# Kernel optimization log

Measured on AMD Instinct MI355X. Metric: run time of the kernel, lower is better.

Reference implementation:

```python
import jax, jax.numpy as jnp
import numpy as np

B, N, C, H, D = 1, 4096, 256, 8, 64  # batch, seq, channels, heads, head_dim


def setup_inputs() -> dict:
    key = jax.random.key(0)
    ks = jax.random.split(key, 11)
    s = 0.02
    return {
        "q_x": jax.random.normal(ks[0], (B, N, C), jnp.float32),
        "k_x": jax.random.normal(ks[1], (B, N, C), jnp.float32),
        "v_x": jax.random.normal(ks[2], (B, N, C), jnp.float32),
        "bias": jax.random.normal(ks[3], (B, 1, N, N), jnp.float32),
        "wq": jax.random.normal(ks[4], (H * D, C), jnp.float32) * s,
        "wk": jax.random.normal(ks[5], (H * D, C), jnp.float32) * s,
        "wv": jax.random.normal(ks[6], (H * D, C), jnp.float32) * s,
        "wg": jax.random.normal(ks[7], (H * D, C), jnp.float32) * s,
        "bg": jnp.ones((H * D,), jnp.float32),  # gating bias init = 1
        "wo": jax.random.normal(ks[8], (C, H * D), jnp.float32) * s,
        "bo": jnp.zeros((C,), jnp.float32),
        "q_chunk_size": 256,
        "kv_chunk_size": 1024,
    }


def reference(q_x, k_x, v_x, bias, wq, wk, wv, wg, bg, wo, bo,
              q_chunk_size, kv_chunk_size):
    # The chunked Rabe-Staats loop computes exact softmax attention; the
    # chunk sizes are memory knobs only, so the reference computes the
    # mathematically identical full attention.
    q = (q_x @ wq.T).reshape(*q_x.shape[:-1], H, D) / jnp.sqrt(jnp.asarray(D, q_x.dtype))
    k = (k_x @ wk.T).reshape(*k_x.shape[:-1], H, D)
    v = (v_x @ wv.T).reshape(*v_x.shape[:-1], H, D)
    logits = jnp.einsum("bqhd,bkhd->bhqk", q, k) + bias  # [B,H,Q,K]
    p = jax.nn.softmax(logits, axis=-1)
    o = jnp.einsum("bkhd,bhqk->bqhd", v, p)  # [B,Q,H,D]
    g = jax.nn.sigmoid(q_x @ wg.T + bg).reshape(*q_x.shape[:-1], H, D)
    o = o * g
    o = o.reshape(*o.shape[:-2], H * D)
    return o @ wo.T + bo
```

## Files before the change

### kernel.cpp

```cpp
#include <hip/hip_runtime.h>
#include <stdint.h>

#define NN 4096
#define CC 256
#define HD 512
#define DD 64
#define KSPLIT 3

typedef __attribute__((ext_vector_type(8))) short short8;
typedef __attribute__((ext_vector_type(4))) float floatx4;

__device__ __forceinline__ unsigned short f2bf(float x) {
    union { float f; unsigned int u; } v; v.f = x;
    unsigned int u = v.u + 0x7fffu + ((v.u >> 16) & 1u);
    return (unsigned short)(u >> 16);
}
__device__ __forceinline__ float bf2f(unsigned short s) {
    union { unsigned int u; float f; } v; v.u = ((unsigned int)s) << 16;
    return v.f;
}

#if defined(__has_builtin) && __has_builtin(__builtin_amdgcn_cvt_pk_bf16_f32)
typedef __attribute__((ext_vector_type(2))) __bf16 bf16x2_t;
__device__ __forceinline__ unsigned int pack2bf(float a, float b) {
    union { bf16x2_t v; unsigned int u; } x;
    x.v = __builtin_amdgcn_cvt_pk_bf16_f32(a, b);
    return x.u;
}
#else
__device__ __forceinline__ unsigned int pack2bf(float a, float b) {
    return ((unsigned int)f2bf(b) << 16) | (unsigned int)f2bf(a);
}
#endif

#define GLOAD_LDS(gp, lp) __builtin_amdgcn_global_load_lds(                    \
    (__attribute__((address_space(1))) void*)(gp),                             \
    (__attribute__((address_space(3))) void*)(lp), 16, 0, 0)

__global__ __launch_bounds__(256) void prep_kernel(
    const float* __restrict__ qx, const float* __restrict__ kx,
    const float* __restrict__ vx,
    const float* __restrict__ wq, const float* __restrict__ wk,
    const float* __restrict__ wv, const float* __restrict__ wg,
    const float* __restrict__ wo,
    unsigned short* __restrict__ qxb, unsigned short* __restrict__ kxb,
    unsigned short* __restrict__ vxb, unsigned short* __restrict__ Wb,
    unsigned short* __restrict__ wob)
{
    const int z = blockIdx.y;
    const float* src; unsigned short* dst; int n; float s = 1.0f;
    switch (z) {
        case 0: src = qx; dst = qxb; n = NN * CC; break;
        case 1: src = kx; dst = kxb; n = NN * CC; break;
        case 2: src = vx; dst = vxb; n = NN * CC; break;
        case 3: src = wq; dst = Wb;               n = HD * CC; s = 0.125f; break;
        case 4: src = wk; dst = Wb + 1 * HD * CC; n = HD * CC; break;
        case 5: src = wv; dst = Wb + 2 * HD * CC; n = HD * CC; break;
        case 6: src = wg; dst = Wb + 3 * HD * CC; n = HD * CC; break;
        default: src = wo; dst = wob;             n = CC * HD; break;
    }
    int i = (blockIdx.x * 256 + threadIdx.x) * 4;
    if (i < n) {
        float4 v = *(const float4*)&src[i];
        ushort4 p;
        p.x = f2bf(v.x * s); p.y = f2bf(v.y * s);
        p.z = f2bf(v.z * s); p.w = f2bf(v.w * s);
        *(ushort4*)&dst[i] = p;
    }
}

__global__ __launch_bounds__(256, 4) void proj_kernel(
    const unsigned short* __restrict__ qxb, const unsigned short* __restrict__ kxb,
    const unsigned short* __restrict__ vxb, const unsigned short* __restrict__ Wb,
    const float* __restrict__ bg,
    unsigned short* __restrict__ Qb, unsigned short* __restrict__ Kb,
    unsigned short* __restrict__ VbT, unsigned short* __restrict__ Gb)
{
    const int m0 = blockIdx.x * 128;
    const int nb = blockIdx.y;
    const int n0 = nb * 128;
    const int mode = nb >> 2;
    const unsigned short* X = (mode == 1) ? kxb : (mode == 2) ? vxb : qxb;

    const int tid = threadIdx.x;
    const int wid = tid >> 6;
    const int wr = wid >> 1, wc = wid & 1;
    const int lane = tid & 63;
    const int quad = lane >> 4;
    const int ln = lane & 15;
    const int lnx = ln & 7;

    __shared__ __align__(16) unsigned short smem[128 * 136];
    unsigned short* Xs = smem;
    unsigned short* Ws = smem + 128 * 64;

    floatx4 acc[4][4] = {};

    for (int k0 = 0; k0 < CC; k0 += 64) {
        #pragma unroll
        for (int t = 0; t < 4; t++) {
            int row = wid * 32 + t * 8 + (lane >> 3);
            int c = (lane & 7) ^ (lane >> 3);
            GLOAD_LDS(&X[(size_t)(m0 + row) * CC + k0 + c * 8],
                      &Xs[(wid * 32 + t * 8) * 64]);
            GLOAD_LDS(&Wb[(size_t)(n0 + row) * CC + k0 + c * 8],
                      &Ws[(wid * 32 + t * 8) * 64]);
        }
        __syncthreads();

        #pragma unroll
        for (int ks = 0; ks < 64; ks += 32) {
            const int cb = ks >> 3;
            short8 a[4], b[4];
            #pragma unroll
            for (int i = 0; i < 4; i++)
                a[i] = *(const short8*)&Xs[(wr * 64 + i * 16 + ln) * 64 +
                                           (((quad ^ cb) ^ lnx) * 8)];
            #pragma unroll
            for (int j = 0; j < 4; j++)
                b[j] = *(const short8*)&Ws[(wc * 64 + j * 16 + ln) * 64 +
                                           (((quad ^ cb) ^ lnx) * 8)];
            #pragma unroll
            for (int i = 0; i < 4; i++)
                #pragma unroll
                for (int j = 0; j < 4; j++)
                    acc[i][j] = __builtin_amdgcn_mfma_f32_16x16x32_bf16(a[i], b[j], acc[i][j], 0, 0, 0);
        }
        __syncthreads();
    }

    const int subn = nb & 3;
    if (mode != 2) {
        unsigned short* Out = (mode == 0) ? Qb : (mode == 1) ? Kb : Gb;
        #pragma unroll
        for (int i = 0; i < 4; i++) {
            #pragma unroll
            for (int j = 0; j < 4; j++) {
                int col = subn * 128 + wc * 64 + j * 16 + ln;
                float bgv = (mode == 3) ? bg[col] : 0.0f;
                #pragma unroll
                for (int r = 0; r < 4; r++) {
                    int row = m0 + wr * 64 + i * 16 + quad * 4 + r;
                    float v = acc[i][j][r];
                    if (mode == 3) v = 1.0f / (1.0f + __expf(-(v + bgv)));
                    Out[(size_t)row * HD + col] = f2bf(v);
                }
            }
        }
    } else {
        #pragma unroll
        for (int i = 0; i < 4; i++) {
            #pragma unroll
            for (int j = 0; j < 4; j++) {
                int cl = wc * 64 + j * 16 + ln;
                #pragma unroll
                for (int r = 0; r < 4; r++) {
                    int rl = wr * 64 + i * 16 + quad * 4 + r;
                    smem[cl * 136 + rl] = f2bf(acc[i][j][r]);
                }
            }
        }
        __syncthreads();
        #pragma unroll
        for (int it = 0; it < 8; it++) {
            int idx = it * 256 + tid;
            int c = idx >> 4, ch = idx & 15;
            short8 vv = *(const short8*)&smem[c * 136 + ch * 8];
            *(short8*)&VbT[(size_t)(subn * 128 + c) * NN + m0 + ch * 8] = vv;
        }
    }
}

__global__ __launch_bounds__(256, 6) void attn_kernel(
    const unsigned short* __restrict__ Qb, const unsigned short* __restrict__ Kb,
    const unsigned short* __restrict__ VbT,
    const float* __restrict__ bias,
    unsigned short* __restrict__ Opart, float* __restrict__ Lpart)
{
    const int h = blockIdx.y;
    const int q0 = blockIdx.x * 64;
    const int sp = blockIdx.z;
    const int tbeg = (sp * 64) / KSPLIT;
    const int tend = ((sp + 1) * 64) / KSPLIT;
    const int tid = threadIdx.x;
    const int wid = tid >> 6;
    const int lane = tid & 63;
    const int quad = lane >> 4;
    const int ln = lane & 15;
    const int lnx = ln & 7;

    __shared__ __align__(16) unsigned short Ks[64 * 64];
    __shared__ __align__(16) unsigned short Vs[64 * 64];
    __shared__ __align__(16) unsigned short Ps[64 * 72];

    const int qrow = q0 + wid * 16 + ln;
    short8 qa0 = *(const short8*)&Qb[(size_t)qrow * HD + h * DD + quad * 8];
    short8 qa1 = *(const short8*)&Qb[(size_t)qrow * HD + h * DD + 32 + quad * 8];

    floatx4 O[4] = {};
    float lsum[4] = {0.0f, 0.0f, 0.0f, 0.0f};

    for (int kt = tbeg; kt < tend; kt++) {
        const int k0 = kt * 64;
        #pragma unroll
        for (int t = 0; t < 2; t++) {
            int row = wid * 16 + t * 8 + (lane >> 3);
            int c = (lane & 7) ^ (lane >> 3);
            GLOAD_LDS(&Kb[(size_t)(k0 + row) * HD + h * DD + c * 8],
                      &Ks[(wid * 16 + t * 8) * 64]);
            GLOAD_LDS(&VbT[(size_t)(h * DD + row) * NN + k0 + c * 8],
                      &Vs[(wid * 16 + t * 8) * 64]);
        }

        float bv[4][4];
        #pragma unroll
        for (int r = 0; r < 4; r++) {
            const float* brow = &bias[(size_t)(q0 + wid * 16 + quad * 4 + r) * NN + k0];
            #pragma unroll
            for (int n = 0; n < 4; n++) bv[r][n] = brow[n * 16 + ln];
        }
        __syncthreads();

        floatx4 S[4];
        #pragma unroll
        for (int n = 0; n < 4; n++)
            S[n] = (floatx4){bv[0][n], bv[1][n], bv[2][n], bv[3][n]};
        #pragma unroll
        for (int n = 0; n < 4; n++) {
            short8 b0 = *(const short8*)&Ks[(n * 16 + ln) * 64 + ((quad ^ lnx) * 8)];
            S[n] = __builtin_amdgcn_mfma_f32_16x16x32_bf16(qa0, b0, S[n], 0, 0, 0);
            short8 b1 = *(const short8*)&Ks[(n * 16 + ln) * 64 + (((quad ^ 4) ^ lnx) * 8)];
            S[n] = __builtin_amdgcn_mfma_f32_16x16x32_bf16(qa1, b1, S[n], 0, 0, 0);
        }

        #pragma unroll
        for (int r = 0; r < 4; r++) {
            int prow = (wid * 16 + quad * 4 + r) * 72;
            #pragma unroll
            for (int n = 0; n < 4; n += 2) {
                float p0 = __expf(S[n][r]);
                float p1 = __expf(S[n + 1][r]);
                lsum[r] += p0 + p1;
                unsigned int pk = pack2bf(p0, p1);
                Ps[prow + n * 16 + ln] = (unsigned short)(pk & 0xffffu);
                Ps[prow + (n + 1) * 16 + ln] = (unsigned short)(pk >> 16);
            }
        }

        #pragma unroll
        for (int ks = 0; ks < 64; ks += 32) {
            const int cb = ks >> 3;
            short8 a = *(const short8*)&Ps[(wid * 16 + ln) * 72 + ks + quad * 8];
            #pragma unroll
            for (int nd = 0; nd < 4; nd++) {
                short8 b = *(const short8*)&Vs[(nd * 16 + ln) * 64 +
                                               (((quad ^ cb) ^ lnx) * 8)];
                O[nd] = __builtin_amdgcn_mfma_f32_16x16x32_bf16(a, b, O[nd], 0, 0, 0);
            }
        }
        __syncthreads();
    }

    #pragma unroll
    for (int r = 0; r < 4; r++) {
        #pragma unroll
        for (int off = 1; off < 16; off <<= 1)
            lsum[r] += __shfl_xor(lsum[r], off);
        int grow = q0 + wid * 16 + quad * 4 + r;
        size_t base = ((size_t)(sp * 8 + h) * NN + grow) * 64;
        #pragma unroll
        for (int nd = 0; nd < 4; nd++)
            Opart[base + nd * 16 + ln] = f2bf(O[nd][r]);
        if (ln == 0)
            Lpart[(size_t)(sp * 8 + h) * NN + grow] = lsum[r];
    }
}

__global__ __launch_bounds__(256) void combine_kernel(
    const unsigned short* __restrict__ Opart, const float* __restrict__ Lpart,
    const unsigned short* __restrict__ Gb, unsigned short* __restrict__ OGb)
{
    const int tid = threadIdx.x;
    const int d = tid & 63;
    const int flat = blockIdx.x * 4 + (tid >> 6);
    const int h = flat >> 12;
    const int q = flat & (NN - 1);

    float l = 0.0f, o = 0.0f;
    #pragma unroll
    for (int sp = 0; sp < KSPLIT; sp++) {
        size_t idx = (size_t)(sp * 8 + h) * NN + q;
        l += Lpart[idx];
        o += bf2f(Opart[idx * 64 + d]);
    }
    float inv = 1.0f / l;
    int col = h * DD + d;
    float g = bf2f(Gb[(size_t)q * HD + col]);
    OGb[(size_t)q * HD + col] = f2bf(o * inv * g);
}

__global__ __launch_bounds__(256, 4) void outproj_kernel(
    const unsigned short* __restrict__ OGb, const unsigned short* __restrict__ wob,
    const float* __restrict__ bo, float* __restrict__ out)
{
    const int m0 = blockIdx.x * 64;
    const int n0 = blockIdx.y * 64;
    const int tid = threadIdx.x;
    const int wid = tid >> 6;
    const int lane = tid & 63;
    const int quad = lane >> 4;
    const int ln = lane & 15;
    const int lnx = ln & 7;

    __shared__ __align__(16) unsigned short Xs[64 * 64];
    __shared__ __align__(16) unsigned short Ws[64 * 64];

    floatx4 acc[4] = {};

    for (int k0 = 0; k0 < HD; k0 += 64) {
        #pragma unroll
        for (int t = 0; t < 2; t++) {
            int row = wid * 16 + t * 8 + (lane >> 3);
            int c = (lane & 7) ^ (lane >> 3);
            GLOAD_LDS(&OGb[(size_t)(m0 + row) * HD + k0 + c * 8],
                      &Xs[(wid * 16 + t * 8) * 64]);
            GLOAD_LDS(&wob[(size_t)(n0 + row) * HD + k0 + c * 8],
                      &Ws[(wid * 16 + t * 8) * 64]);
        }
        __syncthreads();

        #pragma unroll
        for (int ks = 0; ks < 64; ks += 32) {
            const int cb = ks >> 3;
            short8 a = *(const short8*)&Xs[(wid * 16 + ln) * 64 +
                                           (((quad ^ cb) ^ lnx) * 8)];
            #pragma unroll
            for (int n = 0; n < 4; n++) {
                short8 b = *(const short8*)&Ws[(n * 16 + ln) * 64 +
                                               (((quad ^ cb) ^ lnx) * 8)];
                acc[n] = __builtin_amdgcn_mfma_f32_16x16x32_bf16(a, b, acc[n], 0, 0, 0);
            }
        }
        __syncthreads();
    }

    #pragma unroll
    for (int n = 0; n < 4; n++) {
        int col = n0 + n * 16 + ln;
        float bov = bo[col];
        #pragma unroll
        for (int r = 0; r < 4; r++) {
            int row = m0 + wid * 16 + quad * 4 + r;
            out[(size_t)row * CC + col] = acc[n][r] + bov;
        }
    }
}

extern "C" void kernel_launch(void* const* d_in, const int* in_sizes, int n_in,
                              void* d_out, int out_size, void* d_ws, size_t ws_size,
                              hipStream_t stream) {
    const float* qx   = (const float*)d_in[0];
    const float* kx   = (const float*)d_in[1];
    const float* vx   = (const float*)d_in[2];
    const float* bias = (const float*)d_in[3];
    const float* wq   = (const float*)d_in[4];
    const float* wk   = (const float*)d_in[5];
    const float* wv   = (const float*)d_in[6];
    const float* wg   = (const float*)d_in[7];
    const float* bg   = (const float*)d_in[8];
    const float* wo   = (const float*)d_in[9];
    const float* bo   = (const float*)d_in[10];
    float* out = (float*)d_out;

    char* ws = (char*)d_ws;
    const size_t MB = (size_t)1 << 20;
    unsigned short* wob   = (unsigned short*)(ws);
    float*          Lpart = (float*)(ws + MB / 4);
    unsigned short* Qb    = (unsigned short*)(ws + 1 * MB);
    unsigned short* Kb    = (unsigned short*)(ws + 5 * MB);
    unsigned short* VbT   = (unsigned short*)(ws + 9 * MB);
    unsigned short* Gb    = (unsigned short*)(ws + 13 * MB);
    unsigned short* OGb   = (unsigned short*)(ws + 17 * MB);
    unsigned short* qxb   = (unsigned short*)(ws + 21 * MB);
    unsigned short* kxb   = (unsigned short*)(ws + 23 * MB);
    unsigned short* vxb   = (unsigned short*)(ws + 25 * MB);
    unsigned short* Wb    = (unsigned short*)(ws + 27 * MB);
    unsigned short* Opart = (unsigned short*)(ws + 21 * MB);

    prep_kernel<<<dim3(NN * CC / (256 * 4), 8), 256, 0, stream>>>(
        qx, kx, vx, wq, wk, wv, wg, wo, qxb, kxb, vxb, Wb, wob);
    proj_kernel<<<dim3(32, 16), 256, 0, stream>>>(
        qxb, kxb, vxb, Wb, bg, Qb, Kb, VbT, Gb);
    attn_kernel<<<dim3(64, 8, KSPLIT), 256, 0, stream>>>(
        Qb, Kb, VbT, bias, Opart, Lpart);
    combine_kernel<<<dim3(NN * 8 / 4), 256, 0, stream>>>(
        Opart, Lpart, Gb, OGb);
    outproj_kernel<<<dim3(64, 4), 256, 0, stream>>>(
        OGb, wob, bo, out);
}
```

Measured before the change: 210.8 us.

## Double-buffer K/V tiles and prefetch bias in attention, split KV in two

The attention kernel now double-buffers the K and V LDS tiles and register-prefetches the next tile's bias while computing the current one, so there is one barrier per iteration instead of two. The KV split drops from 3 to 2 with a fixed 32-tile loop, and occupancy hints drop from 6 to 4 blocks. The P scratch buffer uses an XOR swizzle instead of padding, and s_setprio is raised around the MFMA sections. These changes aim to hide global-load latency, at the cost of more LDS and registers per block and fewer parallel blocks.

New measurement: 214.4 us. Within noise of the previous version (+1.7%).

```diff
diff --git a/kernel.cpp b/kernel.cpp
--- a/kernel.cpp
+++ b/kernel.cpp
@@ -5,7 +5,7 @@
 #define CC 256
 #define HD 512
 #define DD 64
-#define KSPLIT 3
+#define KSPLIT 2
 
 typedef __attribute__((ext_vector_type(8))) short short8;
 typedef __attribute__((ext_vector_type(4))) float floatx4;
@@ -171,7 +171,7 @@
     }
 }
 
-__global__ __launch_bounds__(256, 6) void attn_kernel(
+__global__ __launch_bounds__(256, 4) void attn_kernel(
     const unsigned short* __restrict__ Qb, const unsigned short* __restrict__ Kb,
     const unsigned short* __restrict__ VbT,
     const float* __restrict__ bias,
@@ -180,18 +180,19 @@
     const int h = blockIdx.y;
     const int q0 = blockIdx.x * 64;
     const int sp = blockIdx.z;
-    const int tbeg = (sp * 64) / KSPLIT;
-    const int tend = ((sp + 1) * 64) / KSPLIT;
+    const int tbeg = sp * 32;
     const int tid = threadIdx.x;
     const int wid = tid >> 6;
     const int lane = tid & 63;
     const int quad = lane >> 4;
     const int ln = lane & 15;
     const int lnx = ln & 7;
-
-    __shared__ __align__(16) unsigned short Ks[64 * 64];
-    __shared__ __align__(16) unsigned short Vs[64 * 64];
-    __shared__ __align__(16) unsigned short Ps[64 * 72];
+    const int hi3 = (ln >> 3) << 3;
+    const int sc = (lane & 7) ^ (lane >> 3);
+
+    __shared__ __align__(16) unsigned short Ks[2][64 * 64];
+    __shared__ __align__(16) unsigned short Vs[2][64 * 64];
+    __shared__ __align__(16) unsigned short Ps[64 * 64];
 
     const int qrow = q0 + wid * 16 + ln;
     short8 qa0 = *(const short8*)&Qb[(size_t)qrow * HD + h * DD + quad * 8];
@@ -200,66 +201,95 @@
     floatx4 O[4] = {};
     float lsum[4] = {0.0f, 0.0f, 0.0f, 0.0f};
 
-    for (int kt = tbeg; kt < tend; kt++) {
-        const int k0 = kt * 64;
+    auto STAGE = [&](int kt, int bf) {
+        const size_t k0 = (size_t)kt * 64;
         #pragma unroll
         for (int t = 0; t < 2; t++) {
             int row = wid * 16 + t * 8 + (lane >> 3);
-            int c = (lane & 7) ^ (lane >> 3);
-            GLOAD_LDS(&Kb[(size_t)(k0 + row) * HD + h * DD + c * 8],
-                      &Ks[(wid * 16 + t * 8) * 64]);
-            GLOAD_LDS(&VbT[(size_t)(h * DD + row) * NN + k0 + c * 8],
-                      &Vs[(wid * 16 + t * 8) * 64]);
-        }
-
-        float bv[4][4];
+            GLOAD_LDS(&Kb[(k0 + row) * HD + h * DD + sc * 8],
+                      &Ks[bf][(wid * 16 + t * 8) * 64]);
+            GLOAD_LDS(&VbT[(size_t)(h * DD + row) * NN + k0 + sc * 8],
+                      &Vs[bf][(wid * 16 + t * 8) * 64]);
+        }
+    };
+
+    const float* bbase = &bias[(size_t)(q0 + wid * 16 + quad * 4) * NN + ln];
+    auto LBIAS = [&](int kt, float (&bv)[4][4]) {
+        #pragma unroll
+        for (int r = 0; r < 4; r++)
+            #pragma unroll
+            for (int n = 0; n < 4; n++)
+                bv[r][n] = bbase[(size_t)r * NN + kt * 64 + n * 16];
+    };
+
+    float bvA[4][4], bvB[4][4];
+
+    STAGE(tbeg, 0);
+    LBIAS(tbeg, bvA);
+    __syncthreads();
+
+    auto ITER = [&](int kt, int bf, float (&bvC)[4][4], float (&bvN)[4][4],
+                    bool pre) {
+        if (pre) {
+            STAGE(kt + 1, bf ^ 1);
+            LBIAS(kt + 1, bvN);
+        }
+
+        floatx4 S[4];
+        #pragma unroll
+        for (int n = 0; n < 4; n++)
+            S[n] = (floatx4){bvC[0][n], bvC[1][n], bvC[2][n], bvC[3][n]};
+        __builtin_amdgcn_s_setprio(1);
+        #pragma unroll
+        for (int n = 0; n < 4; n++) {
+            short8 b0 = *(const short8*)&Ks[bf][(n * 16 + ln) * 64 + ((quad ^ lnx) * 8)];
+            S[n] = __builtin_amdgcn_mfma_f32_16x16x32_bf16(qa0, b0, S[n], 0, 0, 0);
+            short8 b1 = *(const short8*)&Ks[bf][(n * 16 + ln) * 64 + (((quad ^ 4) ^ lnx) * 8)];
+            S[n] = __builtin_amdgcn_mfma_f32_16x16x32_bf16(qa1, b1, S[n], 0, 0, 0);
+        }
+        __builtin_amdgcn_s_setprio(0);
+
         #pragma unroll
         for (int r = 0; r < 4; r++) {
-            const float* brow = &bias[(size_t)(q0 + wid * 16 + quad * 4 + r) * NN + k0];
-            #pragma unroll
-            for (int n = 0; n < 4; n++) bv[r][n] = brow[n * 16 + ln];
-        }
-        __syncthreads();
-
-        floatx4 S[4];
-        #pragma unroll
-        for (int n = 0; n < 4; n++)
-            S[n] = (floatx4){bv[0][n], bv[1][n], bv[2][n], bv[3][n]};
-        #pragma unroll
-        for (int n = 0; n < 4; n++) {
-            short8 b0 = *(const short8*)&Ks[(n * 16 + ln) * 64 + ((quad ^ lnx) * 8)];
-            S[n] = __builtin_amdgcn_mfma_f32_16x16x32_bf16(qa0, b0, S[n], 0, 0, 0);
-            short8 b1 = *(const short8*)&Ks[(n * 16 + ln) * 64 + (((quad ^ 4) ^ lnx) * 8)];
-            S[n] = __builtin_amdgcn_mfma_f32_16x16x32_bf16(qa1, b1, S[n], 0, 0, 0);
-        }
-
-        #pragma unroll
-        for (int r = 0; r < 4; r++) {
-            int prow = (wid * 16 + quad * 4 + r) * 72;
+            int prow = wid * 16 + quad * 4 + r;
+            int pb = (prow * 64 + lnx) ^ ((prow & 7) << 3) ^ hi3;
             #pragma unroll
             for (int n = 0; n < 4; n += 2) {
                 float p0 = __expf(S[n][r]);
                 float p1 = __expf(S[n + 1][r]);
                 lsum[r] += p0 + p1;
                 unsigned int pk = pack2bf(p0, p1);
-                Ps[prow + n * 16 + ln] = (unsigned short)(pk & 0xffffu);
-                Ps[prow + (n + 1) * 16 + ln] = (unsigned short)(pk >> 16);
+                Ps[pb ^ (n << 4)] = (unsigned short)(pk & 0xffffu);
+                Ps[pb ^ ((n + 1) << 4)] = (unsigned short)(pk >> 16);
             }
         }
 
+        __builtin_amdgcn_s_setprio(1);
         #pragma unroll
         for (int ks = 0; ks < 64; ks += 32) {
             const int cb = ks >> 3;
-            short8 a = *(const short8*)&Ps[(wid * 16 + ln) * 72 + ks + quad * 8];
+            short8 a = *(const short8*)&Ps[(wid * 16 + ln) * 64 +
+                                           (((cb | quad) ^ lnx) * 8)];
             #pragma unroll
             for (int nd = 0; nd < 4; nd++) {
-                short8 b = *(const short8*)&Vs[(nd * 16 + ln) * 64 +
-                                               (((quad ^ cb) ^ lnx) * 8)];
-                O[nd] = __builtin_amdgcn_mfma_f32_16x16x32_bf16(a, b, O[nd], 0, 0, 0);
+                short8 vb = *(const short8*)&Vs[bf][(nd * 16 + ln) * 64 +
+                                                    (((quad ^ cb) ^ lnx) * 8)];
+                O[nd] = __builtin_amdgcn_mfma_f32_16x16x32_bf16(a, vb, O[nd], 0, 0, 0);
             }
         }
-        __syncthreads();
-    }
+        __builtin_amdgcn_s_setprio(0);
+
+        if (pre)
+            __syncthreads();
+    };
+
+    #pragma unroll 1
+    for (int i = 0; i < 30; i += 2) {
+        ITER(tbeg + i,     0, bvA, bvB, true);
+        ITER(tbeg + i + 1, 1, bvB, bvA, true);
+    }
+    ITER(tbeg + 30, 0, bvA, bvB, true);
+    ITER(tbeg + 31, 1, bvB, bvA, false);
 
     #pragma unroll
     for (int r = 0; r < 4; r++) {
```

## Keep P in registers by transposing QK^T MFMA and using 16x16x16 PV MFMA

Applied to the files above, without the earlier changes.

The QK^T MFMA operands are swapped so each lane holds four consecutive key columns of one query row. That lets the exponentiated probabilities feed a 16x16x16 bf16 MFMA directly from registers, removing the Ps shared-memory round trip and its LDS writes and reads. Bias is now loaded as float4 per lane instead of scalar gathers, and the row-sum reduction shrinks to two shuffles. It also adds s_setprio around the MFMA blocks, and the PV step uses twice as many smaller MFMA instructions, so there is some added issue overhead.

Result: slower. 235.6 us (+11.7%).

```diff
diff --git a/kernel.cpp b/kernel.cpp
--- a/kernel.cpp
+++ b/kernel.cpp
@@ -8,6 +8,7 @@
 #define KSPLIT 3
 
 typedef __attribute__((ext_vector_type(8))) short short8;
+typedef __attribute__((ext_vector_type(4))) short short4v;
 typedef __attribute__((ext_vector_type(4))) float floatx4;
 
 __device__ __forceinline__ unsigned short f2bf(float x) {
@@ -30,6 +31,17 @@
 #else
 __device__ __forceinline__ unsigned int pack2bf(float a, float b) {
     return ((unsigned int)f2bf(b) << 16) | (unsigned int)f2bf(a);
+}
+#endif
+
+#if defined(__has_builtin) && __has_builtin(__builtin_amdgcn_mfma_f32_16x16x16bf16_1k)
+__device__ __forceinline__ floatx4 mfma16(short4v a, short4v b, floatx4 c) {
+    return __builtin_amdgcn_mfma_f32_16x16x16bf16_1k(a, b, c, 0, 0, 0);
+}
+#else
+__device__ __forceinline__ floatx4 mfma16(short4v a, short4v b, floatx4 c) {
+    asm("v_mfma_f32_16x16x16_bf16 %0, %1, %2, %0" : "+v"(c) : "v"(a), "v"(b));
+    return c;
 }
 #endif
 
@@ -188,92 +200,91 @@
     const int quad = lane >> 4;
     const int ln = lane & 15;
     const int lnx = ln & 7;
+    const int sc = (lane & 7) ^ (lane >> 3);
 
     __shared__ __align__(16) unsigned short Ks[64 * 64];
     __shared__ __align__(16) unsigned short Vs[64 * 64];
-    __shared__ __align__(16) unsigned short Ps[64 * 72];
 
     const int qrow = q0 + wid * 16 + ln;
     short8 qa0 = *(const short8*)&Qb[(size_t)qrow * HD + h * DD + quad * 8];
     short8 qa1 = *(const short8*)&Qb[(size_t)qrow * HD + h * DD + 32 + quad * 8];
 
     floatx4 O[4] = {};
-    float lsum[4] = {0.0f, 0.0f, 0.0f, 0.0f};
+    float lsum = 0.0f;
+
+    const float* bbase = &bias[(size_t)qrow * NN + quad * 4];
 
     for (int kt = tbeg; kt < tend; kt++) {
         const int k0 = kt * 64;
         #pragma unroll
         for (int t = 0; t < 2; t++) {
             int row = wid * 16 + t * 8 + (lane >> 3);
-            int c = (lane & 7) ^ (lane >> 3);
-            GLOAD_LDS(&Kb[(size_t)(k0 + row) * HD + h * DD + c * 8],
+            GLOAD_LDS(&Kb[(size_t)(k0 + row) * HD + h * DD + sc * 8],
                       &Ks[(wid * 16 + t * 8) * 64]);
-            GLOAD_LDS(&VbT[(size_t)(h * DD + row) * NN + k0 + c * 8],
+            GLOAD_LDS(&VbT[(size_t)(h * DD + row) * NN + k0 + sc * 8],
                       &Vs[(wid * 16 + t * 8) * 64]);
         }
 
-        float bv[4][4];
-        #pragma unroll
-        for (int r = 0; r < 4; r++) {
-            const float* brow = &bias[(size_t)(q0 + wid * 16 + quad * 4 + r) * NN + k0];
-            #pragma unroll
-            for (int n = 0; n < 4; n++) bv[r][n] = brow[n * 16 + ln];
-        }
-        __syncthreads();
-
         floatx4 S[4];
         #pragma unroll
-        for (int n = 0; n < 4; n++)
-            S[n] = (floatx4){bv[0][n], bv[1][n], bv[2][n], bv[3][n]};
+        for (int n = 0; n < 4; n++) {
+            float4 b4 = *(const float4*)&bbase[k0 + n * 16];
+            S[n] = (floatx4){b4.x, b4.y, b4.z, b4.w};
+        }
+        __syncthreads();
+
+        __builtin_amdgcn_s_setprio(1);
         #pragma unroll
         for (int n = 0; n < 4; n++) {
             short8 b0 = *(const short8*)&Ks[(n * 16 + ln) * 64 + ((quad ^ lnx) * 8)];
-            S[n] = __builtin_amdgcn_mfma_f32_16x16x32_bf16(qa0, b0, S[n], 0, 0, 0);
+            S[n] = __builtin_amdgcn_mfma_f32_16x16x32_bf16(b0, qa0, S[n], 0, 0, 0);
             short8 b1 = *(const short8*)&Ks[(n * 16 + ln) * 64 + (((quad ^ 4) ^ lnx) * 8)];
-            S[n] = __builtin_amdgcn_mfma_f32_16x16x32_bf16(qa1, b1, S[n], 0, 0, 0);
-        }
-
-        #pragma unroll
-        for (int r = 0; r < 4; r++) {
-            int prow = (wid * 16 + quad * 4 + r) * 72;
-            #pragma unroll
-            for (int n = 0; n < 4; n += 2) {
-                float p0 = __expf(S[n][r]);
-                float p1 = __expf(S[n + 1][r]);
-                lsum[r] += p0 + p1;
-                unsigned int pk = pack2bf(p0, p1);
-                Ps[prow + n * 16 + ln] = (unsigned short)(pk & 0xffffu);
-                Ps[prow + (n + 1) * 16 + ln] = (unsigned short)(pk >> 16);
+            S[n] = __builtin_amdgcn_mfma_f32_16x16x32_bf16(b1, qa1, S[n], 0, 0, 0);
+        }
+        __builtin_amdgcn_s_setprio(0);
+
+        short4v pa[4];
+        #pragma unroll
+        for (int n = 0; n < 4; n++) {
+            float p0 = __expf(S[n][0]);
+            float p1 = __expf(S[n][1]);
+            float p2 = __expf(S[n][2]);
+            float p3 = __expf(S[n][3]);
+            lsum += (p0 + p1) + (p2 + p3);
+            union { unsigned int u[2]; short4v s; } pk;
+            pk.u[0] = pack2bf(p0, p1);
+            pk.u[1] = pack2bf(p2, p3);
+            pa[n] = pk.s;
+        }
+
+        __builtin_amdgcn_s_setprio(1);
+        #pragma unroll
+        for (int n = 0; n < 4; n++) {
+            #pragma unroll
+            for (int nd = 0; nd < 4; nd++) {
+                const int ch = (n * 2 + (quad >> 1)) ^ lnx;
+                short4v vb = *(const short4v*)&Vs[(nd * 16 + ln) * 64 +
+                                                  ch * 8 + (quad & 1) * 4];
+                O[nd] = mfma16(pa[n], vb, O[nd]);
             }
         }
-
-        #pragma unroll
-        for (int ks = 0; ks < 64; ks += 32) {
-            const int cb = ks >> 3;
-            short8 a = *(const short8*)&Ps[(wid * 16 + ln) * 72 + ks + quad * 8];
-            #pragma unroll
-            for (int nd = 0; nd < 4; nd++) {
-                short8 b = *(const short8*)&Vs[(nd * 16 + ln) * 64 +
-                                               (((quad ^ cb) ^ lnx) * 8)];
-                O[nd] = __builtin_amdgcn_mfma_f32_16x16x32_bf16(a, b, O[nd], 0, 0, 0);
-            }
-        }
-        __syncthreads();
-    }
+        __builtin_amdgcn_s_setprio(0);
+        __syncthreads();
+    }
+
+    lsum += __shfl_xor(lsum, 16);
+    lsum += __shfl_xor(lsum, 32);
 
     #pragma unroll
     for (int r = 0; r < 4; r++) {
-        #pragma unroll
-        for (int off = 1; off < 16; off <<= 1)
-            lsum[r] += __shfl_xor(lsum[r], off);
         int grow = q0 + wid * 16 + quad * 4 + r;
         size_t base = ((size_t)(sp * 8 + h) * NN + grow) * 64;
         #pragma unroll
         for (int nd = 0; nd < 4; nd++)
             Opart[base + nd * 16 + ln] = f2bf(O[nd][r]);
-        if (ln == 0)
-            Lpart[(size_t)(sp * 8 + h) * NN + grow] = lsum[r];
-    }
+    }
+    if (lane < 16)
+        Lpart[(size_t)(sp * 8 + h) * NN + qrow] = lsum;
 }
 
 __global__ __launch_bounds__(256) void combine_kernel(
```

## Fuse split-K combine and gating into outproj; raise KSPLIT and shrink P buffer

Applied to the files above, without the earlier changes.

Removes the separate combine kernel. The output projection now sums the KSPLIT partial O and L values, normalises, applies the sigmoid gate and writes the bf16 tile straight into shared memory. The attention kernel moves to 4 KV splits with 8 blocks per CU and processes P in two 32-column halves in a smaller swizzled Ps buffer, which cuts LDS use per block. This saves one launch and a global round-trip of the gated output. In exchange, outproj recomputes the combine per N-tile (4 times) and holds more partial buffers.

New measurement: 279.7 us. +32.7%, slower.

```diff
diff --git a/kernel.cpp b/kernel.cpp
--- a/kernel.cpp
+++ b/kernel.cpp
@@ -5,7 +5,7 @@
 #define CC 256
 #define HD 512
 #define DD 64
-#define KSPLIT 3
+#define KSPLIT 4
 
 typedef __attribute__((ext_vector_type(8))) short short8;
 typedef __attribute__((ext_vector_type(4))) float floatx4;
@@ -171,7 +171,7 @@
     }
 }
 
-__global__ __launch_bounds__(256, 6) void attn_kernel(
+__global__ __launch_bounds__(256, 8) void attn_kernel(
     const unsigned short* __restrict__ Qb, const unsigned short* __restrict__ Kb,
     const unsigned short* __restrict__ VbT,
     const float* __restrict__ bias,
@@ -180,18 +180,19 @@
     const int h = blockIdx.y;
     const int q0 = blockIdx.x * 64;
     const int sp = blockIdx.z;
-    const int tbeg = (sp * 64) / KSPLIT;
-    const int tend = ((sp + 1) * 64) / KSPLIT;
+    const int tbeg = sp * 16;
+    const int tend = tbeg + 16;
     const int tid = threadIdx.x;
     const int wid = tid >> 6;
     const int lane = tid & 63;
     const int quad = lane >> 4;
     const int ln = lane & 15;
     const int lnx = ln & 7;
+    const int sc = (lane & 7) ^ (lane >> 3);
 
     __shared__ __align__(16) unsigned short Ks[64 * 64];
     __shared__ __align__(16) unsigned short Vs[64 * 64];
-    __shared__ __align__(16) unsigned short Ps[64 * 72];
+    __shared__ __align__(16) unsigned short Ps[64 * 32];
 
     const int qrow = q0 + wid * 16 + ln;
     short8 qa0 = *(const short8*)&Qb[(size_t)qrow * HD + h * DD + quad * 8];
@@ -205,10 +206,9 @@
         #pragma unroll
         for (int t = 0; t < 2; t++) {
             int row = wid * 16 + t * 8 + (lane >> 3);
-            int c = (lane & 7) ^ (lane >> 3);
-            GLOAD_LDS(&Kb[(size_t)(k0 + row) * HD + h * DD + c * 8],
+            GLOAD_LDS(&Kb[(size_t)(k0 + row) * HD + h * DD + sc * 8],
                       &Ks[(wid * 16 + t * 8) * 64]);
-            GLOAD_LDS(&VbT[(size_t)(h * DD + row) * NN + k0 + c * 8],
+            GLOAD_LDS(&VbT[(size_t)(h * DD + row) * NN + k0 + sc * 8],
                       &Vs[(wid * 16 + t * 8) * 64]);
         }
 
@@ -234,23 +234,26 @@
         }
 
         #pragma unroll
-        for (int r = 0; r < 4; r++) {
-            int prow = (wid * 16 + quad * 4 + r) * 72;
-            #pragma unroll
-            for (int n = 0; n < 4; n += 2) {
-                float p0 = __expf(S[n][r]);
-                float p1 = __expf(S[n + 1][r]);
+        for (int half = 0; half < 2; half++) {
+            const int nlo = half * 2;
+            #pragma unroll
+            for (int r = 0; r < 4; r++) {
+                const int prow = wid * 16 + quad * 4 + r;
+                const int rx = (prow >> 1) & 3;
+                const int pb = prow * 32 + (ln & 7);
+                float p0 = __expf(S[nlo][r]);
+                float p1 = __expf(S[nlo + 1][r]);
                 lsum[r] += p0 + p1;
                 unsigned int pk = pack2bf(p0, p1);
-                Ps[prow + n * 16 + ln] = (unsigned short)(pk & 0xffffu);
-                Ps[prow + (n + 1) * 16 + ln] = (unsigned short)(pk >> 16);
-            }
-        }
-
-        #pragma unroll
-        for (int ks = 0; ks < 64; ks += 32) {
+                const int c0 = ln >> 3;
+                Ps[pb + (((c0) ^ rx) * 8)]     = (unsigned short)(pk & 0xffffu);
+                Ps[pb + (((2 + c0) ^ rx) * 8)] = (unsigned short)(pk >> 16);
+            }
+            const int ks = half * 32;
             const int cb = ks >> 3;
-            short8 a = *(const short8*)&Ps[(wid * 16 + ln) * 72 + ks + quad * 8];
+            const int arow = wid * 16 + ln;
+            short8 a = *(const short8*)&Ps[arow * 32 +
+                                           ((quad ^ ((arow >> 1) & 3)) * 8)];
             #pragma unroll
             for (int nd = 0; nd < 4; nd++) {
                 short8 b = *(const short8*)&Vs[(nd * 16 + ln) * 64 +
@@ -276,31 +279,9 @@
     }
 }
 
-__global__ __launch_bounds__(256) void combine_kernel(
+__global__ __launch_bounds__(256, 4) void outproj_kernel(
     const unsigned short* __restrict__ Opart, const float* __restrict__ Lpart,
-    const unsigned short* __restrict__ Gb, unsigned short* __restrict__ OGb)
-{
-    const int tid = threadIdx.x;
-    const int d = tid & 63;
-    const int flat = blockIdx.x * 4 + (tid >> 6);
-    const int h = flat >> 12;
-    const int q = flat & (NN - 1);
-
-    float l = 0.0f, o = 0.0f;
-    #pragma unroll
-    for (int sp = 0; sp < KSPLIT; sp++) {
-        size_t idx = (size_t)(sp * 8 + h) * NN + q;
-        l += Lpart[idx];
-        o += bf2f(Opart[idx * 64 + d]);
-    }
-    float inv = 1.0f / l;
-    int col = h * DD + d;
-    float g = bf2f(Gb[(size_t)q * HD + col]);
-    OGb[(size_t)q * HD + col] = f2bf(o * inv * g);
-}
-
-__global__ __launch_bounds__(256, 4) void outproj_kernel(
-    const unsigned short* __restrict__ OGb, const unsigned short* __restrict__ wob,
+    const unsigned short* __restrict__ Gb, const unsigned short* __restrict__ wob,
     const float* __restrict__ bo, float* __restrict__ out)
 {
     const int m0 = blockIdx.x * 64;
@@ -317,15 +298,38 @@
 
     floatx4 acc[4] = {};
 
-    for (int k0 = 0; k0 < HD; k0 += 64) {
+    for (int h = 0; h < 8; h++) {
         #pragma unroll
         for (int t = 0; t < 2; t++) {
             int row = wid * 16 + t * 8 + (lane >> 3);
             int c = (lane & 7) ^ (lane >> 3);
-            GLOAD_LDS(&OGb[(size_t)(m0 + row) * HD + k0 + c * 8],
-                      &Xs[(wid * 16 + t * 8) * 64]);
-            GLOAD_LDS(&wob[(size_t)(n0 + row) * HD + k0 + c * 8],
+            GLOAD_LDS(&wob[(size_t)(n0 + row) * HD + h * 64 + c * 8],
                       &Ws[(wid * 16 + t * 8) * 64]);
+        }
+        #pragma unroll
+        for (int t = 0; t < 2; t++) {
+            int row = wid * 16 + t * 8 + (lane >> 3);
+            int q = m0 + row;
+            int c = (lane & 7) ^ (lane >> 3);
+            int d0 = c * 8;
+            float l = 0.0f;
+            float ov[8] = {};
+            #pragma unroll
+            for (int sp = 0; sp < KSPLIT; sp++) {
+                size_t idx = (size_t)(sp * 8 + h) * NN + q;
+                l += Lpart[idx];
+                short8 o8 = *(const short8*)&Opart[idx * 64 + d0];
+                #pragma unroll
+                for (int j = 0; j < 8; j++) ov[j] += bf2f((unsigned short)o8[j]);
+            }
+            float inv = 1.0f / l;
+            short8 g8 = *(const short8*)&Gb[(size_t)q * HD + h * 64 + d0];
+            union { unsigned int u[4]; short8 s; } pk;
+            #pragma unroll
+            for (int j = 0; j < 4; j++)
+                pk.u[j] = pack2bf(ov[2 * j] * inv * bf2f((unsigned short)g8[2 * j]),
+                                  ov[2 * j + 1] * inv * bf2f((unsigned short)g8[2 * j + 1]));
+            *(short8*)&Xs[(size_t)row * 64 + (lane & 7) * 8] = pk.s;
         }
         __syncthreads();
 
@@ -380,12 +384,11 @@
     unsigned short* Kb    = (unsigned short*)(ws + 5 * MB);
     unsigned short* VbT   = (unsigned short*)(ws + 9 * MB);
     unsigned short* Gb    = (unsigned short*)(ws + 13 * MB);
-    unsigned short* OGb   = (unsigned short*)(ws + 17 * MB);
     unsigned short* qxb   = (unsigned short*)(ws + 21 * MB);
     unsigned short* kxb   = (unsigned short*)(ws + 23 * MB);
     unsigned short* vxb   = (unsigned short*)(ws + 25 * MB);
     unsigned short* Wb    = (unsigned short*)(ws + 27 * MB);
-    unsigned short* Opart = (unsigned short*)(ws + 21 * MB);
+    unsigned short* Opart = (unsigned short*)(ws + 17 * MB);
 
     prep_kernel<<<dim3(NN * CC / (256 * 4), 8), 256, 0, stream>>>(
         qx, kx, vx, wq, wk, wv, wg, wo, qxb, kxb, vxb, Wb, wob);
@@ -393,8 +396,6 @@
         qxb, kxb, vxb, Wb, bg, Qb, Kb, VbT, Gb);
     attn_kernel<<<dim3(64, 8, KSPLIT), 256, 0, stream>>>(
         Qb, Kb, VbT, bias, Opart, Lpart);
-    combine_kernel<<<dim3(NN * 8 / 4), 256, 0, stream>>>(
-        Opart, Lpart, Gb, OGb);
     outproj_kernel<<<dim3(64, 4), 256, 0, stream>>>(
-        OGb, wob, bo, out);
-}
+        Opart, Lpart, Gb, wob, bo, out);
+}
```
